# Kernel tuning notes

Measured on AMD Instinct MI355X. Metric: run time of the kernel, lower is better.

Reference implementation:

```python
import jax, jax.numpy as jnp
import numpy as np

SEQ, BSZ, D = 1024, 16, 512
HEADS = 8
DEG = 32
N = SEQ * BSZ
E = N * DEG
NEG_SLOPE = 0.2  # PyG GATConv leaky_relu slope


def setup_inputs() -> dict:
    key = jax.random.key(0)
    ks = jax.random.split(key, 12)
    x = jax.random.normal(ks[0], (SEQ, BSZ, D), dtype=jnp.float32)
    # per-graph random COO edges, node ids offset per graph (PyG Batch semantics)
    src = jax.random.randint(ks[1], (BSZ, SEQ * DEG), 0, SEQ)
    dst = jax.random.randint(ks[2], (BSZ, SEQ * DEG), 0, SEQ)
    off = (jnp.arange(BSZ) * SEQ)[:, None]
    edge_index = jnp.stack([(src + off).reshape(-1), (dst + off).reshape(-1)]).astype(jnp.int32)  # [2, E]
    s = 0.05
    W0 = jax.random.normal(ks[3], (D, D), dtype=jnp.float32) * s          # heads*64 = 512
    att_src0 = jax.random.normal(ks[4], (HEADS, 64), dtype=jnp.float32) * s
    att_dst0 = jax.random.normal(ks[5], (HEADS, 64), dtype=jnp.float32) * s
    b0 = jax.random.normal(ks[6], (D,), dtype=jnp.float32) * s
    W1 = jax.random.normal(ks[7], (D, HEADS * D), dtype=jnp.float32) * s  # concat=False layer
    att_src1 = jax.random.normal(ks[8], (HEADS, D), dtype=jnp.float32) * s
    att_dst1 = jax.random.normal(ks[9], (HEADS, D), dtype=jnp.float32) * s
    b1 = jax.random.normal(ks[10], (D,), dtype=jnp.float32) * s
    return {"x": x, "edge_index": edge_index, "W0": W0, "att_src0": att_src0,
            "att_dst0": att_dst0, "b0": b0, "W1": W1, "att_src1": att_src1,
            "att_dst1": att_dst1, "b1": b1}


def gat_conv(h_in, src, dst, n_nodes, W, a_src, a_dst, b, concat):
    """PyG GATConv (eval mode: no dropout). src/dst already include self-loops."""
    H, C = a_src.shape
    h = (h_in @ W).reshape(n_nodes, H, C)                     # [N,H,C]
    alpha_src = jnp.einsum('nhc,hc->nh', h, a_src)            # [N,H]
    alpha_dst = jnp.einsum('nhc,hc->nh', h, a_dst)
    e = jax.nn.leaky_relu(alpha_src[src] + alpha_dst[dst], NEG_SLOPE)  # [Etot,H]
    # segment softmax over incoming edges of each dst node
    m = jax.ops.segment_max(e, dst, num_segments=n_nodes)
    m = jnp.where(jnp.isfinite(m), m, 0.0)
    p = jnp.exp(e - m[dst])
    z = jax.ops.segment_sum(p, dst, num_segments=n_nodes)
    alpha = p / (z[dst] + 1e-16)                              # [Etot,H]
    msg = h[src] * alpha[:, :, None]                          # [Etot,H,C]
    out = jax.ops.segment_sum(msg, dst, num_segments=n_nodes) # [N,H,C]
    out = out.reshape(n_nodes, H * C) if concat else out.mean(axis=1)
    return out + b


def reference(x, edge_index, W0, att_src0, att_dst0, b0, W1, att_src1, att_dst1, b1):
    seq_len, bsz, d = x.shape
    n_nodes = seq_len * bsz
    # PyG Batch: graph n contributes x[:, n, :] as its node block
    nodes = jnp.transpose(x, (1, 0, 2)).reshape(n_nodes, d)
    # GATConv add_self_loops=True
    loop = jnp.arange(n_nodes, dtype=edge_index.dtype)
    src = jnp.concatenate([edge_index[0], loop])
    dst = jnp.concatenate([edge_index[1], loop])
    h = jax.nn.elu(gat_conv(nodes, src, dst, n_nodes, W0, att_src0, att_dst0, b0, concat=True))
    h = jax.nn.elu(gat_conv(h, src, dst, n_nodes, W1, att_src1, att_dst1, b1, concat=False))
    # original code: conv_x.view(seq_len, bsz, embed_dim)  (raw memory reinterpret)
    return h.reshape(seq_len, bsz, d)
```

## Files before the change

kernel.cpp:

```cpp
#include <hip/hip_runtime.h>
#include <hip/hip_bf16.h>


#define NNODES 16384
#define MXIT 12

typedef unsigned short u16;
typedef unsigned int u32;
typedef __attribute__((ext_vector_type(8))) __bf16 bf16x8;
typedef __attribute__((ext_vector_type(4))) float f32x4;

__device__ __forceinline__ u16 f2bf(float v) {
    u32 u = __builtin_bit_cast(u32, v);
    u32 r = (u + 0x7fffu + ((u >> 16) & 1u)) >> 16;
    return (u16)r;
}
__device__ __forceinline__ float bf2f(u16 s) {
    u32 u = ((u32)s) << 16;
    return __builtin_bit_cast(float, u);
}
__device__ __forceinline__ float bflo(u32 u) {
    return __builtin_bit_cast(float, u << 16);
}
__device__ __forceinline__ float bfhi(u32 u) {
    return __builtin_bit_cast(float, u & 0xffff0000u);
}
__device__ __forceinline__ void split2(float v, u16& h, u16& l) {
    h = f2bf(v);
    l = f2bf(v - bf2f(h));
}
__device__ __forceinline__ u32 pack2(float a, float b) {
    return (u32)f2bf(a) | ((u32)f2bf(b) << 16);
}

__device__ __forceinline__ void gload_lds16(const u16* g, u16* l) {
    __builtin_amdgcn_global_load_lds(
        (__attribute__((address_space(1))) void*)(void*)(g),
        (__attribute__((address_space(3))) void*)(void*)(l), 16, 0, 0);
}

__global__ void zero_k(int* p, int n) {
    int i = blockIdx.x * 256 + threadIdx.x;
    if (i < n) p[i] = 0;
}

__global__ void count_k(const int* __restrict__ dst, int E, int* __restrict__ deg) {
    int i = blockIdx.x * 256 + threadIdx.x;
    if (i < E) atomicAdd(&deg[dst[i]], 1);
}

__global__ __launch_bounds__(1024) void scan_k(const int* __restrict__ deg,
                                               int* __restrict__ indptr,
                                               int* __restrict__ cursor, int n) {
    __shared__ int sums[1024];
    int t = threadIdx.x;
    int base = t * 16;
    int local[16];
    int s = 0;
    #pragma unroll
    for (int i = 0; i < 16; i++) { local[i] = s; s += deg[base + i]; }
    sums[t] = s;
    __syncthreads();
    for (int off = 1; off < 1024; off <<= 1) {
        int v = (t >= off) ? sums[t - off] : 0;
        __syncthreads();
        sums[t] += v;
        __syncthreads();
    }
    int base_sum = (t == 0) ? 0 : sums[t - 1];
    #pragma unroll
    for (int i = 0; i < 16; i++) {
        int v = base_sum + local[i];
        indptr[base + i] = v;
        cursor[base + i] = v;
    }
    if (t == 1023) indptr[n] = base_sum + s;
}

__global__ void scatter_k(const int* __restrict__ src, const int* __restrict__ dst,
                          int E, int* __restrict__ cursor, int* __restrict__ csr) {
    int i = blockIdx.x * 256 + threadIdx.x;
    if (i < E) {
        int pos = atomicAdd(&cursor[dst[i]], 1);
        csr[pos] = src[i];
    }
}

__global__ void prepx_k(const float* __restrict__ x, u16* __restrict__ xh,
                        u16* __restrict__ xl) {
    int idx = blockIdx.x * 256 + threadIdx.x;
    int e = idx << 2;
    int n = e >> 9, k = e & 511;
    int g = n >> 10, s = n & 1023;
    float4 v = *(const float4*)(x + ((size_t)(s * 16 + g) << 9) + k);
    u16 h[4], l[4];
    split2(v.x, h[0], l[0]);
    split2(v.y, h[1], l[1]);
    split2(v.z, h[2], l[2]);
    split2(v.w, h[3], l[3]);
    size_t o = ((size_t)n << 9) + k;
    *(ushort4*)(xh + o) = make_ushort4(h[0], h[1], h[2], h[3]);
    *(ushort4*)(xl + o) = make_ushort4(l[0], l[1], l[2], l[3]);
}

__global__ __launch_bounds__(256) void prepW0t_k(const float* __restrict__ W0,
                                                 u16* __restrict__ Wh,
                                                 u16* __restrict__ Wl) {
    __shared__ u32 tile[64][65];
    int b = blockIdx.x;
    int kt = (b >> 3) * 64, nt = (b & 7) * 64;
    int t = threadIdx.x;
    #pragma unroll
    for (int i = 0; i < 16; i++) {
        int idx = i * 256 + t;
        int r = idx >> 6, c = idx & 63;
        float v = W0[(size_t)(kt + r) * 512 + nt + c];
        u16 h, l;
        split2(v, h, l);
        tile[r][c] = ((u32)h << 16) | l;
    }
    __syncthreads();
    #pragma unroll
    for (int i = 0; i < 8; i++) {
        int idx = i * 256 + t;
        int r = idx >> 5, c2 = (idx & 31) * 2;
        u32 p0 = tile[c2][r], p1 = tile[c2 + 1][r];
        size_t o = (size_t)(nt + r) * 512 + kt + c2;
        *(ushort2*)(Wh + o) = make_ushort2((u16)(p0 >> 16), (u16)(p1 >> 16));
        *(ushort2*)(Wl + o) = make_ushort2((u16)(p0 & 0xffff), (u16)(p1 & 0xffff));
    }
}

__global__ __launch_bounds__(256) void prepW1t_k(const float* __restrict__ W1,
                                                 u16* __restrict__ Bh) {
    __shared__ u16 tile[64][66];
    int b = blockIdx.x;
    int hh = b >> 6;
    int rem = b & 63;
    int kt = (rem >> 3) * 64, ct = (rem & 7) * 64;
    int t = threadIdx.x;
    #pragma unroll
    for (int i = 0; i < 16; i++) {
        int idx = i * 256 + t;
        int r = idx >> 6, c = idx & 63;
        float v = W1[(size_t)(kt + r) * 4096 + hh * 512 + ct + c] * 0.125f;
        tile[r][c] = f2bf(v);
    }
    __syncthreads();
    #pragma unroll
    for (int i = 0; i < 8; i++) {
        int idx = i * 256 + t;
        int r = idx >> 5, c2 = (idx & 31) * 2;
        size_t o = (size_t)(ct + r) * 4096 + hh * 512 + kt + c2;
        *(ushort2*)(Bh + o) = make_ushort2(tile[c2][r], tile[c2 + 1][r]);
    }
}

template <int MODE, int TERMS>
__global__ __launch_bounds__(256) void mgemm_k(
    const u16* __restrict__ Ah, const u16* __restrict__ Al,
    const u16* __restrict__ Bh, const u16* __restrict__ Bl,
    void* __restrict__ Cv, int K, const float* __restrict__ bias,
    const float* __restrict__ att_s, const float* __restrict__ att_d,
    float* __restrict__ as_, float* __restrict__ ad_) {
    __shared__ u16 smem[16384];

    int t = threadIdx.x;
    int lane = t & 63, w = t >> 6;
    int wr = w >> 1, wc = w & 1;

    int orig = blockIdx.x + (blockIdx.y << 2);
    int xcd = orig & 7, slot = orig >> 3;
    int by = xcd * ((int)gridDim.y >> 3) + (slot >> 2);
    int bx = slot & 3;
    int row0 = by * 128, col0 = bx * 128;

    f32x4 acc[4][4];
    #pragma unroll
    for (int i = 0; i < 4; i++)
        #pragma unroll
        for (int j = 0; j < 4; j++) acc[i][j] = (f32x4){0.f, 0.f, 0.f, 0.f};

    int srow = lane >> 2;
    int sl4 = lane & 3;
    const u16* gp[8];
    u16* lp[8];
    #pragma unroll
    for (int ii = 0; ii < 8; ii++) {
        const u16* gb;
        int g0, koff;
        if (TERMS == 3) {
            gb = (w == 0) ? Ah : (w == 1) ? Al : (w == 2) ? Bh : Bl;
            g0 = (w < 2) ? row0 : col0;
            koff = 0;
        } else {
            gb = (w < 2) ? Ah : Bh;
            g0 = (w < 2) ? row0 : col0;
            koff = (w & 1) * 32;
        }
        int row = ii * 16 + srow;
        int sslot = sl4 ^ ((row >> 1) & 3);
        gp[ii] = gb + (size_t)(g0 + row) * K + koff + sslot * 8;
        lp[ii] = smem + w * 4096 + ii * 512;
    }

    int rl = lane & 15, kb = lane >> 4;

    if (TERMS == 3) {
        for (int k0 = 0; k0 < K; k0 += 32) {
            #pragma unroll
            for (int ii = 0; ii < 8; ii++) gload_lds16(gp[ii] + k0, lp[ii]);
            __syncthreads();

            bf16x8 afh[4], afl_[4], bfh[4], bfl[4];
            #pragma unroll
            for (int f = 0; f < 4; f++) {
                int r = wr * 64 + f * 16 + rl;
                int off = r * 32 + ((kb ^ ((r >> 1) & 3)) << 3);
                afh[f] = *(const bf16x8*)(smem + off);
                afl_[f] = *(const bf16x8*)(smem + 4096 + off);
            }
            #pragma unroll
            for (int j = 0; j < 4; j++) {
                int r = wc * 64 + j * 16 + rl;
                int off = r * 32 + ((kb ^ ((r >> 1) & 3)) << 3);
                bfh[j] = *(const bf16x8*)(smem + 8192 + off);
                bfl[j] = *(const bf16x8*)(smem + 12288 + off);
            }
            #pragma unroll
            for (int i = 0; i < 4; i++)
                #pragma unroll
                for (int j = 0; j < 4; j++) {
                    acc[i][j] = __builtin_amdgcn_mfma_f32_16x16x32_bf16(
                        afl_[i], bfh[j], acc[i][j], 0, 0, 0);
                    acc[i][j] = __builtin_amdgcn_mfma_f32_16x16x32_bf16(
                        afh[i], bfl[j], acc[i][j], 0, 0, 0);
                    acc[i][j] = __builtin_amdgcn_mfma_f32_16x16x32_bf16(
                        afh[i], bfh[j], acc[i][j], 0, 0, 0);
                }
            __syncthreads();
        }
    } else {
        for (int k0 = 0; k0 < K; k0 += 64) {
            #pragma unroll
            for (int ii = 0; ii < 8; ii++) gload_lds16(gp[ii] + k0, lp[ii]);
            __syncthreads();

            #pragma unroll
            for (int ks = 0; ks < 2; ks++) {
                bf16x8 af[4], bf[4];
                #pragma unroll
                for (int f = 0; f < 4; f++) {
                    int r = wr * 64 + f * 16 + rl;
                    int off = r * 32 + ((kb ^ ((r >> 1) & 3)) << 3);
                    af[f] = *(const bf16x8*)(smem + ks * 4096 + off);
                }
                #pragma unroll
                for (int j = 0; j < 4; j++) {
                    int r = wc * 64 + j * 16 + rl;
                    int off = r * 32 + ((kb ^ ((r >> 1) & 3)) << 3);
                    bf[j] = *(const bf16x8*)(smem + 8192 + ks * 4096 + off);
                }
                #pragma unroll
                for (int i = 0; i < 4; i++)
                    #pragma unroll
                    for (int j = 0; j < 4; j++)
                        acc[i][j] = __builtin_amdgcn_mfma_f32_16x16x32_bf16(
                            af[i], bf[j], acc[i][j], 0, 0, 0);
            }
            __syncthreads();
        }
    }

    int cr = kb * 4;
    #pragma unroll
    for (int i = 0; i < 4; i++) {
        #pragma unroll
        for (int j = 0; j < 4; j++) {
            int col = col0 + wc * 64 + j * 16 + rl;
            float bv = (MODE == 1) ? bias[col] : 0.f;
            f32x4 v = acc[i][j];
            #pragma unroll
            for (int q = 0; q < 4; q++) {
                float o = v[q] + bv;
                size_t grow = (size_t)(row0 + wr * 64 + i * 16 + cr + q);
                if (MODE == 1) {
                    o = o > 0.f ? o : __expf(o) - 1.f;
                    ((float*)Cv)[grow * 512 + col] = o;
                } else {
                    ((u16*)Cv)[grow * 512 + col] = f2bf(o);
                }
            }
        }
    }

    if (MODE == 2) {
        int h = (col0 >> 6) + wc;
        float as_v[4], ad_v[4];
        #pragma unroll
        for (int j = 0; j < 4; j++) {
            as_v[j] = att_s[h * 64 + j * 16 + rl];
            ad_v[j] = att_d[h * 64 + j * 16 + rl];
        }
        #pragma unroll
        for (int i = 0; i < 4; i++) {
            float ps[4] = {}, pd[4] = {};
            #pragma unroll
            for (int j = 0; j < 4; j++) {
                f32x4 v = acc[i][j];
                #pragma unroll
                for (int q = 0; q < 4; q++) {
                    ps[q] = fmaf(v[q], as_v[j], ps[q]);
                    pd[q] = fmaf(v[q], ad_v[j], pd[q]);
                }
            }
            #pragma unroll
            for (int off = 1; off < 16; off <<= 1) {
                #pragma unroll
                for (int q = 0; q < 4; q++) {
                    ps[q] += __shfl_xor(ps[q], off);
                    pd[q] += __shfl_xor(pd[q], off);
                }
            }
            if (rl == 0) {
                #pragma unroll
                for (int q = 0; q < 4; q++) {
                    size_t row = (size_t)(row0 + wr * 64 + i * 16 + cr + q);
                    as_[row * 8 + h] = ps[q];
                    ad_[row * 8 + h] = pd[q];
                }
            }
        }
    }
}

__global__ __launch_bounds__(256) void prep1_k(const float* __restrict__ W1,
                                               const float* __restrict__ as1,
                                               const float* __restrict__ ad1,
                                               float* __restrict__ ws1,
                                               float* __restrict__ wd1) {
    int k = blockIdx.x;
    int t = threadIdx.x;
    int h = t >> 5, lane = t & 31;
    float ps = 0.f, pd = 0.f;
    for (int c = lane; c < 512; c += 32) {
        float w = W1[(size_t)k * 4096 + h * 512 + c];
        ps += w * as1[h * 512 + c];
        pd += w * ad1[h * 512 + c];
    }
    #pragma unroll
    for (int off = 1; off < 32; off <<= 1) {
        ps += __shfl_xor(ps, off);
        pd += __shfl_xor(pd, off);
    }
    if (lane == 0) {
        ws1[k * 8 + h] = ps;
        wd1[k * 8 + h] = pd;
    }
}

__global__ __launch_bounds__(256) void node0w_k(
    const u16* __restrict__ h0b, const float* __restrict__ asrc,
    const float* __restrict__ adst, const int* __restrict__ indptr,
    const int* __restrict__ csr, const float* __restrict__ b0,
    const float* __restrict__ ws1, const float* __restrict__ wd1,
    u16* __restrict__ hl0b, float* __restrict__ as1, float* __restrict__ ad1) {
    __shared__ float al_s[4][64];
    __shared__ float red_s[4][16][68];
    int b = blockIdx.x;
    int wid = threadIdx.x >> 6;
    int l = threadIdx.x & 63;
    int d = (b & 7) * (NNODES / 8) + ((b >> 3) << 2) + wid;
    int h = l >> 3;
    int str = l & 7;
    int e0 = indptr[d];
    int ne = indptr[d + 1] - e0;
    float adh = adst[d * 8 + h];

    int svs[MXIT];
    float vs[MXIT];
    #pragma unroll
    for (int ii = 0; ii < MXIT; ii++) {
        int e = str + ii * 8;
        if (e <= ne) svs[ii] = (e < ne) ? csr[e0 + e] : d;
    }
    #pragma unroll
    for (int ii = 0; ii < MXIT; ii++) {
        int e = str + ii * 8;
        if (e <= ne) {
            float v = asrc[svs[ii] * 8 + h] + adh;
            vs[ii] = v > 0.f ? v : 0.2f * v;
        }
    }
    float m = -3.0e38f;
    #pragma unroll
    for (int ii = 0; ii < MXIT; ii++)
        if (str + ii * 8 <= ne) m = fmaxf(m, vs[ii]);
    for (int e = str + MXIT * 8; e <= ne; e += 8) {
        int s = (e < ne) ? csr[e0 + e] : d;
        float v = asrc[s * 8 + h] + adh;
        v = v > 0.f ? v : 0.2f * v;
        m = fmaxf(m, v);
    }
    #pragma unroll
    for (int off = 1; off < 8; off <<= 1) m = fmaxf(m, __shfl_xor(m, off));
    float z = 0.f;
    #pragma unroll
    for (int ii = 0; ii < MXIT; ii++) {
        if (str + ii * 8 <= ne) {
            vs[ii] = __expf(vs[ii] - m);
            z += vs[ii];
        }
    }
    for (int e = str + MXIT * 8; e <= ne; e += 8) {
        int s = (e < ne) ? csr[e0 + e] : d;
        float v = asrc[s * 8 + h] + adh;
        v = v > 0.f ? v : 0.2f * v;
        z += __expf(v - m);
    }
    #pragma unroll
    for (int off = 1; off < 8; off <<= 1) z += __shfl_xor(z, off);
    float rz = 1.0f / (z + 1e-16f);

    float acc[8] = {};
    #pragma unroll
    for (int ii = 0; ii < MXIT; ii++) {
        int eb = ii * 8;
        if (eb <= ne) {
            al_s[wid][str * 8 + h] = vs[ii] * rz;
            int nn = min(8, ne + 1 - eb);
            int sv = svs[ii];
            #pragma unroll
            for (int i = 0; i < 8; i++) {
                if (i < nn) {
                    int s = __shfl(sv, (l & 56) | i);
                    float a = al_s[wid][i * 8 + h];
                    int4 pv = *(const int4*)(h0b + ((size_t)s << 9) + 8 * l);
                    acc[0] = fmaf(a, bflo(pv.x), acc[0]);
                    acc[1] = fmaf(a, bfhi(pv.x), acc[1]);
                    acc[2] = fmaf(a, bflo(pv.y), acc[2]);
                    acc[3] = fmaf(a, bfhi(pv.y), acc[3]);
                    acc[4] = fmaf(a, bflo(pv.z), acc[4]);
                    acc[5] = fmaf(a, bfhi(pv.z), acc[5]);
                    acc[6] = fmaf(a, bflo(pv.w), acc[6]);
                    acc[7] = fmaf(a, bfhi(pv.w), acc[7]);
                }
            }
        }
    }
    for (int eb = MXIT * 8; eb <= ne; eb += 8) {
        int idx = eb + str;
        int sv = (idx < ne) ? csr[e0 + idx] : d;
        {
            float v = asrc[sv * 8 + h] + adh;
            v = v > 0.f ? v : 0.2f * v;
            al_s[wid][str * 8 + h] = __expf(v - m) * rz;
        }
        int nn = min(8, ne + 1 - eb);
        #pragma unroll
        for (int i = 0; i < 8; i++) {
            if (i < nn) {
                int s = __shfl(sv, (l & 56) | i);
                float a = al_s[wid][i * 8 + h];
                int4 pv = *(const int4*)(h0b + ((size_t)s << 9) + 8 * l);
                acc[0] = fmaf(a, bflo(pv.x), acc[0]);
                acc[1] = fmaf(a, bfhi(pv.x), acc[1]);
                acc[2] = fmaf(a, bflo(pv.y), acc[2]);
                acc[3] = fmaf(a, bfhi(pv.y), acc[3]);
                acc[4] = fmaf(a, bflo(pv.z), acc[4]);
                acc[5] = fmaf(a, bfhi(pv.z), acc[5]);
                acc[6] = fmaf(a, bflo(pv.w), acc[6]);
                acc[7] = fmaf(a, bfhi(pv.w), acc[7]);
            }
        }
    }

    const float4* b4 = (const float4*)(b0 + 8 * l);
    float4 bva = b4[0], bvb = b4[1];
    float o[8];
    o[0] = acc[0] + bva.x; o[1] = acc[1] + bva.y;
    o[2] = acc[2] + bva.z; o[3] = acc[3] + bva.w;
    o[4] = acc[4] + bvb.x; o[5] = acc[5] + bvb.y;
    o[6] = acc[6] + bvb.z; o[7] = acc[7] + bvb.w;
    #pragma unroll
    for (int k = 0; k < 8; k++) o[k] = o[k] > 0.f ? o[k] : __expf(o[k]) - 1.f;
    int4 hv;
    hv.x = (int)pack2(o[0], o[1]);
    hv.y = (int)pack2(o[2], o[3]);
    hv.z = (int)pack2(o[4], o[5]);
    hv.w = (int)pack2(o[6], o[7]);
    *(int4*)(hl0b + ((size_t)d << 9) + 8 * l) = hv;

    float ps[8] = {}, pd[8] = {};
    #pragma unroll
    for (int k = 0; k < 8; k++) {
        const float4* w4 = (const float4*)(ws1 + (size_t)(8 * l + k) * 8);
        const float4* v4 = (const float4*)(wd1 + (size_t)(8 * l + k) * 8);
        float4 wa = w4[0], wb = w4[1];
        float4 va = v4[0], vb = v4[1];
        float ok = o[k];
        ps[0] = fmaf(ok, wa.x, ps[0]); ps[1] = fmaf(ok, wa.y, ps[1]);
        ps[2] = fmaf(ok, wa.z, ps[2]); ps[3] = fmaf(ok, wa.w, ps[3]);
        ps[4] = fmaf(ok, wb.x, ps[4]); ps[5] = fmaf(ok, wb.y, ps[5]);
        ps[6] = fmaf(ok, wb.z, ps[6]); ps[7] = fmaf(ok, wb.w, ps[7]);
        pd[0] = fmaf(ok, va.x, pd[0]); pd[1] = fmaf(ok, va.y, pd[1]);
        pd[2] = fmaf(ok, va.z, pd[2]); pd[3] = fmaf(ok, va.w, pd[3]);
        pd[4] = fmaf(ok, vb.x, pd[4]); pd[5] = fmaf(ok, vb.y, pd[5]);
        pd[6] = fmaf(ok, vb.z, pd[6]); pd[7] = fmaf(ok, vb.w, pd[7]);
    }
    #pragma unroll
    for (int j = 0; j < 8; j++) {
        red_s[wid][j][l] = ps[j];
        red_s[wid][8 + j][l] = pd[j];
    }
    if (l < 16) {
        const float4* row = (const float4*)&red_s[wid][l][0];
        float s = 0.f;
        #pragma unroll
        for (int q = 0; q < 16; q++) {
            float4 v = row[q];
            s += (v.x + v.y) + (v.z + v.w);
        }
        if (l < 8) as1[(size_t)d * 8 + l] = s;
        else ad1[(size_t)d * 8 + (l - 8)] = s;
    }
}

__global__ __launch_bounds__(256) void node1w_k(
    const u16* __restrict__ hl0b, const float* __restrict__ asrc,
    const float* __restrict__ adst, const int* __restrict__ indptr,
    const int* __restrict__ csr, u16* __restrict__ aggh, int base, int ch) {
    __shared__ float al_s[4][64];
    int b = blockIdx.x;
    int wid = threadIdx.x >> 6;
    int l = threadIdx.x & 63;
    int dl = (b & 7) * (ch >> 3) + ((b >> 3) << 2) + wid;
    int d = base + dl;
    int hme = l & 7;
    int str = l >> 3;
    int e0 = indptr[d];
    int ne = indptr[d + 1] - e0;
    float adh = adst[d * 8 + hme];

    int svs[MXIT];
    float vs[MXIT];
    #pragma unroll
    for (int ii = 0; ii < MXIT; ii++) {
        int e = str + ii * 8;
        if (e <= ne) svs[ii] = (e < ne) ? csr[e0 + e] : d;
    }
    #pragma unroll
    for (int ii = 0; ii < MXIT; ii++) {
        int e = str + ii * 8;
        if (e <= ne) {
            float v = asrc[svs[ii] * 8 + hme] + adh;
            vs[ii] = v > 0.f ? v : 0.2f * v;
        }
    }
    float m = -3.0e38f;
    #pragma unroll
    for (int ii = 0; ii < MXIT; ii++)
        if (str + ii * 8 <= ne) m = fmaxf(m, vs[ii]);
    for (int e = str + MXIT * 8; e <= ne; e += 8) {
        int s = (e < ne) ? csr[e0 + e] : d;
        float v = asrc[s * 8 + hme] + adh;
        v = v > 0.f ? v : 0.2f * v;
        m = fmaxf(m, v);
    }
    #pragma unroll
    for (int off = 8; off < 64; off <<= 1) m = fmaxf(m, __shfl_xor(m, off));
    float z = 0.f;
    #pragma unroll
    for (int ii = 0; ii < MXIT; ii++) {
        if (str + ii * 8 <= ne) {
            vs[ii] = __expf(vs[ii] - m);
            z += vs[ii];
        }
    }
    for (int e = str + MXIT * 8; e <= ne; e += 8) {
        int s = (e < ne) ? csr[e0 + e] : d;
        float v = asrc[s * 8 + hme] + adh;
        v = v > 0.f ? v : 0.2f * v;
        z += __expf(v - m);
    }
    #pragma unroll
    for (int off = 8; off < 64; off <<= 1) z += __shfl_xor(z, off);
    float rz = 1.0f / (z + 1e-16f);

    float acc[8][8] = {};
    #pragma unroll
    for (int ii = 0; ii < MXIT; ii++) {
        int eb = ii * 8;
        if (eb <= ne) {
            al_s[wid][str * 8 + hme] = vs[ii] * rz;
            int nn = min(8, ne + 1 - eb);
            int sv = svs[ii];
            #pragma unroll
            for (int i = 0; i < 8; i++) {
                if (i < nn) {
                    int s = __shfl(sv, i << 3);
                    const float4* ap = (const float4*)&al_s[wid][i * 8];
                    float4 a0 = ap[0], a1 = ap[1];
                    int4 pv = *(const int4*)(hl0b + ((size_t)s << 9) + 8 * l);
                    float f0 = bflo(pv.x), f1 = bfhi(pv.x);
                    float f2 = bflo(pv.y), f3 = bfhi(pv.y);
                    float f4 = bflo(pv.z), f5 = bfhi(pv.z);
                    float f6 = bflo(pv.w), f7 = bfhi(pv.w);
                    float av[8] = {a0.x, a0.y, a0.z, a0.w,
                                   a1.x, a1.y, a1.z, a1.w};
                    #pragma unroll
                    for (int hh = 0; hh < 8; hh++) {
                        acc[hh][0] = fmaf(av[hh], f0, acc[hh][0]);
                        acc[hh][1] = fmaf(av[hh], f1, acc[hh][1]);
                        acc[hh][2] = fmaf(av[hh], f2, acc[hh][2]);
                        acc[hh][3] = fmaf(av[hh], f3, acc[hh][3]);
                        acc[hh][4] = fmaf(av[hh], f4, acc[hh][4]);
                        acc[hh][5] = fmaf(av[hh], f5, acc[hh][5]);
                        acc[hh][6] = fmaf(av[hh], f6, acc[hh][6]);
                        acc[hh][7] = fmaf(av[hh], f7, acc[hh][7]);
                    }
                }
            }
        }
    }
    for (int eb = MXIT * 8; eb <= ne; eb += 8) {
        int idx = eb + str;
        int sv = (idx < ne) ? csr[e0 + idx] : d;
        {
            float v = asrc[sv * 8 + hme] + adh;
            v = v > 0.f ? v : 0.2f * v;
            al_s[wid][str * 8 + hme] = __expf(v - m) * rz;
        }
        int nn = min(8, ne + 1 - eb);
        #pragma unroll
        for (int i = 0; i < 8; i++) {
            if (i < nn) {
                int s = __shfl(sv, i << 3);
                const float4* ap = (const float4*)&al_s[wid][i * 8];
                float4 a0 = ap[0], a1 = ap[1];
                int4 pv = *(const int4*)(hl0b + ((size_t)s << 9) + 8 * l);
                float f0 = bflo(pv.x), f1 = bfhi(pv.x);
                float f2 = bflo(pv.y), f3 = bfhi(pv.y);
                float f4 = bflo(pv.z), f5 = bfhi(pv.z);
                float f6 = bflo(pv.w), f7 = bfhi(pv.w);
                float av[8] = {a0.x, a0.y, a0.z, a0.w, a1.x, a1.y, a1.z, a1.w};
                #pragma unroll
                for (int hh = 0; hh < 8; hh++) {
                    acc[hh][0] = fmaf(av[hh], f0, acc[hh][0]);
                    acc[hh][1] = fmaf(av[hh], f1, acc[hh][1]);
                    acc[hh][2] = fmaf(av[hh], f2, acc[hh][2]);
                    acc[hh][3] = fmaf(av[hh], f3, acc[hh][3]);
                    acc[hh][4] = fmaf(av[hh], f4, acc[hh][4]);
                    acc[hh][5] = fmaf(av[hh], f5, acc[hh][5]);
                    acc[hh][6] = fmaf(av[hh], f6, acc[hh][6]);
                    acc[hh][7] = fmaf(av[hh], f7, acc[hh][7]);
                }
            }
        }
    }

    #pragma unroll
    for (int hh = 0; hh < 8; hh++) {
        int4 q;
        q.x = (int)(((u32)f2bf(acc[hh][0])) | ((u32)f2bf(acc[hh][1]) << 16));
        q.y = (int)(((u32)f2bf(acc[hh][2])) | ((u32)f2bf(acc[hh][3]) << 16));
        q.z = (int)(((u32)f2bf(acc[hh][4])) | ((u32)f2bf(acc[hh][5]) << 16));
        q.w = (int)(((u32)f2bf(acc[hh][6])) | ((u32)f2bf(acc[hh][7]) << 16));
        size_t ob = (size_t)dl * 4096 + hh * 512 + 8 * l;
        *(int4*)(aggh + ob) = q;
    }
}

extern "C" void kernel_launch(void* const* d_in, const int* in_sizes, int n_in,
                              void* d_out, int out_size, void* d_ws, size_t ws_size,
                              hipStream_t stream) {
    const float* x = (const float*)d_in[0];
    const int* ei = (const int*)d_in[1];
    const float* W0 = (const float*)d_in[2];
    const float* at_s0 = (const float*)d_in[3];
    const float* at_d0 = (const float*)d_in[4];
    const float* b0 = (const float*)d_in[5];
    const float* W1 = (const float*)d_in[6];
    const float* at_s1 = (const float*)d_in[7];
    const float* at_d1 = (const float*)d_in[8];
    const float* b1 = (const float*)d_in[9];
    float* out = (float*)d_out;

    const int N = NNODES;
    const int E = in_sizes[1] / 2;
    const int* esrc = ei;
    const int* edst = ei + E;

    char* p = (char*)d_ws;
    auto carve = [&](size_t bytes) -> void* {
        void* r = (void*)p;
        p += ((bytes + 255) & ~(size_t)255);
        return r;
    };
    u16* h0b = (u16*)carve((size_t)N * 512 * 2);
    u16* hl0b = (u16*)carve((size_t)N * 512 * 2);
    float* as0 = (float*)carve((size_t)N * 8 * 4);
    float* ad0 = (float*)carve((size_t)N * 8 * 4);
    float* as1 = (float*)carve((size_t)N * 8 * 4);
    float* ad1 = (float*)carve((size_t)N * 8 * 4);
    int* deg = (int*)carve((size_t)N * 4);
    int* indptr = (int*)carve((size_t)(N + 1) * 4);
    int* cursor = (int*)carve((size_t)N * 4);
    int* csr = (int*)carve((size_t)E * 4);
    float* ws1 = (float*)carve(512 * 8 * 4);
    float* wd1 = (float*)carve(512 * 8 * 4);
    u16* xh = (u16*)carve((size_t)N * 512 * 2);
    u16* xl = (u16*)carve((size_t)N * 512 * 2);
    u16* W0h = (u16*)carve((size_t)512 * 512 * 2);
    u16* W0l = (u16*)carve((size_t)512 * 512 * 2);
    u16* B1h = (u16*)carve((size_t)512 * 4096 * 2);
    size_t used = (size_t)(p - (char*)d_ws);

    int CH = 1024;
    const int cands[5] = {16384, 8192, 4096, 2048, 1024};
    for (int ci = 0; ci < 5; ci++) {
        if (ws_size >= used + (size_t)cands[ci] * 8192 + 512) {
            CH = cands[ci];
            break;
        }
    }
    u16* aggh = (u16*)carve((size_t)CH * 4096 * 2);

    zero_k<<<(N + 255) / 256, 256, 0, stream>>>(deg, N);
    count_k<<<(E + 255) / 256, 256, 0, stream>>>(edst, E, deg);
    scan_k<<<1, 1024, 0, stream>>>(deg, indptr, cursor, N);
    scatter_k<<<(E + 255) / 256, 256, 0, stream>>>(esrc, edst, E, cursor, csr);

    prepx_k<<<(N * 512 / 4 + 255) / 256, 256, 0, stream>>>(x, xh, xl);
    prepW0t_k<<<64, 256, 0, stream>>>(W0, W0h, W0l);
    prepW1t_k<<<512, 256, 0, stream>>>(W1, B1h);
    prep1_k<<<512, 256, 0, stream>>>(W1, at_s1, at_d1, ws1, wd1);

    mgemm_k<2, 3><<<dim3(4, N / 128), 256, 0, stream>>>(
        xh, xl, W0h, W0l, h0b, 512, nullptr, at_s0, at_d0, as0, ad0);
    node0w_k<<<N / 4, 256, 0, stream>>>(h0b, as0, ad0, indptr, csr, b0, ws1,
                                        wd1, hl0b, as1, ad1);

    for (int base = 0; base < N; base += CH) {
        node1w_k<<<CH / 4, 256, 0, stream>>>(hl0b, as1, ad1, indptr, csr, aggh,
                                             base, CH);
        mgemm_k<1, 1><<<dim3(4, CH / 128), 256, 0, stream>>>(
            aggh, nullptr, B1h, nullptr, out + (size_t)base * 512, 4096, b1,
            nullptr, nullptr, nullptr, nullptr);
    }
}
```

Measured before the change: 385.6 us.

## Split each node's feature gather across two wavefronts in GAT aggregation kernels

Both edge-aggregation kernels now give each destination node to two wavefronts, each covering half of the 512 channels with 8-byte loads instead of 16-byte loads. Grids double and per-thread accumulators halve (node1w goes from 64 to 32 floats), which lowers register pressure and raises occupancy and memory-level parallelism for the irregular gathers. In exchange, the softmax/score computation is done twice per node. node0w also needs a block-wide barrier and a shared-memory reduction across the two halves for the next-layer attention projections.

```diff
diff --git a/kernel.cpp b/kernel.cpp
--- a/kernel.cpp
+++ b/kernel.cpp
@@ -366,16 +366,19 @@
     const float* __restrict__ ws1, const float* __restrict__ wd1,
     u16* __restrict__ hl0b, float* __restrict__ as1, float* __restrict__ ad1) {
     __shared__ float al_s[4][64];
-    __shared__ float red_s[4][16][68];
+    __shared__ float red_s[2][16][136];
     int b = blockIdx.x;
     int wid = threadIdx.x >> 6;
+    int nb = wid >> 1, half = wid & 1;
     int l = threadIdx.x & 63;
-    int d = (b & 7) * (NNODES / 8) + ((b >> 3) << 2) + wid;
-    int h = l >> 3;
+    int d = (b & 7) * (NNODES / 8) + ((b >> 3) << 1) + nb;
+    int hs = l >> 3;
     int str = l & 7;
+    int cb = half * 256 + 4 * l;
+    int ha = cb >> 6;
     int e0 = indptr[d];
     int ne = indptr[d + 1] - e0;
-    float adh = adst[d * 8 + h];
+    float adh = adst[d * 8 + hs];
 
     int svs[MXIT];
     float vs[MXIT];
@@ -388,7 +391,7 @@
     for (int ii = 0; ii < MXIT; ii++) {
         int e = str + ii * 8;
         if (e <= ne) {
-            float v = asrc[svs[ii] * 8 + h] + adh;
+            float v = asrc[svs[ii] * 8 + hs] + adh;
             vs[ii] = v > 0.f ? v : 0.2f * v;
         }
     }
@@ -398,7 +401,7 @@
         if (str + ii * 8 <= ne) m = fmaxf(m, vs[ii]);
     for (int e = str + MXIT * 8; e <= ne; e += 8) {
         int s = (e < ne) ? csr[e0 + e] : d;
-        float v = asrc[s * 8 + h] + adh;
+        float v = asrc[s * 8 + hs] + adh;
         v = v > 0.f ? v : 0.2f * v;
         m = fmaxf(m, v);
     }
@@ -414,7 +417,7 @@
     }
     for (int e = str + MXIT * 8; e <= ne; e += 8) {
         int s = (e < ne) ? csr[e0 + e] : d;
-        float v = asrc[s * 8 + h] + adh;
+        float v = asrc[s * 8 + hs] + adh;
         v = v > 0.f ? v : 0.2f * v;
         z += __expf(v - m);
     }
@@ -422,28 +425,24 @@
     for (int off = 1; off < 8; off <<= 1) z += __shfl_xor(z, off);
     float rz = 1.0f / (z + 1e-16f);
 
-    float acc[8] = {};
+    float acc[4] = {};
     #pragma unroll
     for (int ii = 0; ii < MXIT; ii++) {
         int eb = ii * 8;
         if (eb <= ne) {
-            al_s[wid][str * 8 + h] = vs[ii] * rz;
+            al_s[wid][str * 8 + hs] = vs[ii] * rz;
             int nn = min(8, ne + 1 - eb);
             int sv = svs[ii];
             #pragma unroll
             for (int i = 0; i < 8; i++) {
                 if (i < nn) {
                     int s = __shfl(sv, (l & 56) | i);
-                    float a = al_s[wid][i * 8 + h];
-                    int4 pv = *(const int4*)(h0b + ((size_t)s << 9) + 8 * l);
+                    float a = al_s[wid][i * 8 + ha];
+                    int2 pv = *(const int2*)(h0b + ((size_t)s << 9) + cb);
                     acc[0] = fmaf(a, bflo(pv.x), acc[0]);
                     acc[1] = fmaf(a, bfhi(pv.x), acc[1]);
                     acc[2] = fmaf(a, bflo(pv.y), acc[2]);
                     acc[3] = fmaf(a, bfhi(pv.y), acc[3]);
-                    acc[4] = fmaf(a, bflo(pv.z), acc[4]);
-                    acc[5] = fmaf(a, bfhi(pv.z), acc[5]);
-                    acc[6] = fmaf(a, bflo(pv.w), acc[6]);
-                    acc[7] = fmaf(a, bfhi(pv.w), acc[7]);
                 }
             }
         }
@@ -452,50 +451,41 @@
         int idx = eb + str;
         int sv = (idx < ne) ? csr[e0 + idx] : d;
         {
-            float v = asrc[sv * 8 + h] + adh;
+            float v = asrc[sv * 8 + hs] + adh;
             v = v > 0.f ? v : 0.2f * v;
-            al_s[wid][str * 8 + h] = __expf(v - m) * rz;
+            al_s[wid][str * 8 + hs] = __expf(v - m) * rz;
         }
         int nn = min(8, ne + 1 - eb);
         #pragma unroll
         for (int i = 0; i < 8; i++) {
             if (i < nn) {
                 int s = __shfl(sv, (l & 56) | i);
-                float a = al_s[wid][i * 8 + h];
-                int4 pv = *(const int4*)(h0b + ((size_t)s << 9) + 8 * l);
+                float a = al_s[wid][i * 8 + ha];
+                int2 pv = *(const int2*)(h0b + ((size_t)s << 9) + cb);
                 acc[0] = fmaf(a, bflo(pv.x), acc[0]);
                 acc[1] = fmaf(a, bfhi(pv.x), acc[1]);
                 acc[2] = fmaf(a, bflo(pv.y), acc[2]);
                 acc[3] = fmaf(a, bfhi(pv.y), acc[3]);
-                acc[4] = fmaf(a, bflo(pv.z), acc[4]);
-                acc[5] = fmaf(a, bfhi(pv.z), acc[5]);
-                acc[6] = fmaf(a, bflo(pv.w), acc[6]);
-                acc[7] = fmaf(a, bfhi(pv.w), acc[7]);
-            }
-        }
-    }
-
-    const float4* b4 = (const float4*)(b0 + 8 * l);
-    float4 bva = b4[0], bvb = b4[1];
-    float o[8];
-    o[0] = acc[0] + bva.x; o[1] = acc[1] + bva.y;
-    o[2] = acc[2] + bva.z; o[3] = acc[3] + bva.w;
-    o[4] = acc[4] + bvb.x; o[5] = acc[5] + bvb.y;
-    o[6] = acc[6] + bvb.z; o[7] = acc[7] + bvb.w;
-    #pragma unroll
-    for (int k = 0; k < 8; k++) o[k] = o[k] > 0.f ? o[k] : __expf(o[k]) - 1.f;
-    int4 hv;
+            }
+        }
+    }
+
+    float4 bv = *(const float4*)(b0 + cb);
+    float o[4];
+    o[0] = acc[0] + bv.x; o[1] = acc[1] + bv.y;
+    o[2] = acc[2] + bv.z; o[3] = acc[3] + bv.w;
+    #pragma unroll
+    for (int k = 0; k < 4; k++) o[k] = o[k] > 0.f ? o[k] : __expf(o[k]) - 1.f;
+    int2 hv;
     hv.x = (int)pack2(o[0], o[1]);
     hv.y = (int)pack2(o[2], o[3]);
-    hv.z = (int)pack2(o[4], o[5]);
-    hv.w = (int)pack2(o[6], o[7]);
-    *(int4*)(hl0b + ((size_t)d << 9) + 8 * l) = hv;
+    *(int2*)(hl0b + ((size_t)d << 9) + cb) = hv;
 
     float ps[8] = {}, pd[8] = {};
     #pragma unroll
-    for (int k = 0; k < 8; k++) {
-        const float4* w4 = (const float4*)(ws1 + (size_t)(8 * l + k) * 8);
-        const float4* v4 = (const float4*)(wd1 + (size_t)(8 * l + k) * 8);
+    for (int k = 0; k < 4; k++) {
+        const float4* w4 = (const float4*)(ws1 + (size_t)(cb + k) * 8);
+        const float4* v4 = (const float4*)(wd1 + (size_t)(cb + k) * 8);
         float4 wa = w4[0], wb = w4[1];
         float4 va = v4[0], vb = v4[1];
         float ok = o[k];
@@ -510,19 +500,29 @@
     }
     #pragma unroll
     for (int j = 0; j < 8; j++) {
-        red_s[wid][j][l] = ps[j];
-        red_s[wid][8 + j][l] = pd[j];
-    }
-    if (l < 16) {
-        const float4* row = (const float4*)&red_s[wid][l][0];
+        red_s[nb][j][half * 68 + l] = ps[j];
+        red_s[nb][8 + j][half * 68 + l] = pd[j];
+    }
+    __syncthreads();
+    int t = threadIdx.x;
+    if (t < 32) {
+        int nb2 = t >> 4, j = t & 15;
         float s = 0.f;
+        const float4* r0 = (const float4*)&red_s[nb2][j][0];
         #pragma unroll
         for (int q = 0; q < 16; q++) {
-            float4 v = row[q];
+            float4 v = r0[q];
             s += (v.x + v.y) + (v.z + v.w);
         }
-        if (l < 8) as1[(size_t)d * 8 + l] = s;
-        else ad1[(size_t)d * 8 + (l - 8)] = s;
+        const float4* r1 = (const float4*)&red_s[nb2][j][68];
+        #pragma unroll
+        for (int q = 0; q < 16; q++) {
+            float4 v = r1[q];
+            s += (v.x + v.y) + (v.z + v.w);
+        }
+        int dd = (b & 7) * (NNODES / 8) + ((b >> 3) << 1) + nb2;
+        if (j < 8) as1[(size_t)dd * 8 + j] = s;
+        else ad1[(size_t)dd * 8 + (j - 8)] = s;
     }
 }
 
@@ -533,11 +533,13 @@
     __shared__ float al_s[4][64];
     int b = blockIdx.x;
     int wid = threadIdx.x >> 6;
+    int nb = wid >> 1, half = wid & 1;
     int l = threadIdx.x & 63;
-    int dl = (b & 7) * (ch >> 3) + ((b >> 3) << 2) + wid;
+    int dl = (b & 7) * (ch >> 3) + ((b >> 3) << 1) + nb;
     int d = base + dl;
     int hme = l & 7;
     int str = l >> 3;
+    int cb = half * 256 + 4 * l;
     int e0 = indptr[d];
     int ne = indptr[d + 1] - e0;
     float adh = adst[d * 8 + hme];
@@ -587,7 +589,7 @@
     for (int off = 8; off < 64; off <<= 1) z += __shfl_xor(z, off);
     float rz = 1.0f / (z + 1e-16f);
 
-    float acc[8][8] = {};
+    float acc[8][4] = {};
     #pragma unroll
     for (int ii = 0; ii < MXIT; ii++) {
         int eb = ii * 8;
@@ -601,11 +603,9 @@
                     int s = __shfl(sv, i << 3);
                     const float4* ap = (const float4*)&al_s[wid][i * 8];
                     float4 a0 = ap[0], a1 = ap[1];
-                    int4 pv = *(const int4*)(hl0b + ((size_t)s << 9) + 8 * l);
+                    int2 pv = *(const int2*)(hl0b + ((size_t)s << 9) + cb);
                     float f0 = bflo(pv.x), f1 = bfhi(pv.x);
                     float f2 = bflo(pv.y), f3 = bfhi(pv.y);
-                    float f4 = bflo(pv.z), f5 = bfhi(pv.z);
-                    float f6 = bflo(pv.w), f7 = bfhi(pv.w);
                     float av[8] = {a0.x, a0.y, a0.z, a0.w,
                                    a1.x, a1.y, a1.z, a1.w};
                     #pragma unroll
@@ -614,10 +614,6 @@
                         acc[hh][1] = fmaf(av[hh], f1, acc[hh][1]);
                         acc[hh][2] = fmaf(av[hh], f2, acc[hh][2]);
                         acc[hh][3] = fmaf(av[hh], f3, acc[hh][3]);
-                        acc[hh][4] = fmaf(av[hh], f4, acc[hh][4]);
-                        acc[hh][5] = fmaf(av[hh], f5, acc[hh][5]);
-                        acc[hh][6] = fmaf(av[hh], f6, acc[hh][6]);
-                        acc[hh][7] = fmaf(av[hh], f7, acc[hh][7]);
                     }
                 }
             }
@@ -638,11 +634,9 @@
                 int s = __shfl(sv, i << 3);
                 const float4* ap = (const float4*)&al_s[wid][i * 8];
                 float4 a0 = ap[0], a1 = ap[1];
-                int4 pv = *(const int4*)(hl0b + ((size_t)s << 9) + 8 * l);
+                int2 pv = *(const int2*)(hl0b + ((size_t)s << 9) + cb);
                 float f0 = bflo(pv.x), f1 = bfhi(pv.x);
                 float f2 = bflo(pv.y), f3 = bfhi(pv.y);
-                float f4 = bflo(pv.z), f5 = bfhi(pv.z);
-                float f6 = bflo(pv.w), f7 = bfhi(pv.w);
                 float av[8] = {a0.x, a0.y, a0.z, a0.w, a1.x, a1.y, a1.z, a1.w};
                 #pragma unroll
                 for (int hh = 0; hh < 8; hh++) {
@@ -650,10 +644,6 @@
                     acc[hh][1] = fmaf(av[hh], f1, acc[hh][1]);
                     acc[hh][2] = fmaf(av[hh], f2, acc[hh][2]);
                     acc[hh][3] = fmaf(av[hh], f3, acc[hh][3]);
-                    acc[hh][4] = fmaf(av[hh], f4, acc[hh][4]);
-                    acc[hh][5] = fmaf(av[hh], f5, acc[hh][5]);
-                    acc[hh][6] = fmaf(av[hh], f6, acc[hh][6]);
-                    acc[hh][7] = fmaf(av[hh], f7, acc[hh][7]);
                 }
             }
         }
@@ -661,13 +651,11 @@
 
     #pragma unroll
     for (int hh = 0; hh < 8; hh++) {
-        int4 q;
+        int2 q;
         q.x = (int)(((u32)f2bf(acc[hh][0])) | ((u32)f2bf(acc[hh][1]) << 16));
         q.y = (int)(((u32)f2bf(acc[hh][2])) | ((u32)f2bf(acc[hh][3]) << 16));
-        q.z = (int)(((u32)f2bf(acc[hh][4])) | ((u32)f2bf(acc[hh][5]) << 16));
-        q.w = (int)(((u32)f2bf(acc[hh][6])) | ((u32)f2bf(acc[hh][7]) << 16));
-        size_t ob = (size_t)dl * 4096 + hh * 512 + 8 * l;
-        *(int4*)(aggh + ob) = q;
+        size_t ob = (size_t)dl * 4096 + hh * 512 + cb;
+        *(int2*)(aggh + ob) = q;
     }
 }
 
@@ -738,11 +726,11 @@
 
     mgemm_k<2, 3><<<dim3(4, N / 128), 256, 0, stream>>>(
         xh, xl, W0h, W0l, h0b, 512, nullptr, at_s0, at_d0, as0, ad0);
-    node0w_k<<<N / 4, 256, 0, stream>>>(h0b, as0, ad0, indptr, csr, b0, ws1,
+    node0w_k<<<N / 2, 256, 0, stream>>>(h0b, as0, ad0, indptr, csr, b0, ws1,
                                         wd1, hl0b, as1, ad1);
 
     for (int base = 0; base < N; base += CH) {
-        node1w_k<<<CH / 4, 256, 0, stream>>>(hl0b, as1, ad1, indptr, csr, aggh,
+        node1w_k<<<CH / 2, 256, 0, stream>>>(hl0b, as1, ad1, indptr, csr, aggh,
                                              base, CH);
         mgemm_k<1, 1><<<dim3(4, CH / 128), 256, 0, stream>>>(
             aggh, nullptr, B1h, nullptr, out + (size_t)base * 512, 4096, b1,
```

After: 442.5 us. 14.8% more time.
